# Kernel optimization log

Hardware: AMD Instinct MI355X
Metric: run time of the kernel (lower is better)

The kernel has to match this reference:

```python
import jax, jax.numpy as jnp
import numpy as np
from jax import lax

D, DIM, FF, V, B, S = 8, 1024, 4096, 32000, 2, 2048
EPS = 1e-6

def _rms(x, w):
    return x * lax.rsqrt(jnp.mean(x * x, axis=-1, keepdims=True) + EPS) * w

def _lin(x, W, b):
    # torch nn.Linear: weight [out, in]
    return x @ W.T + b

def _comb(e1, e2):
    # associative op for h_t = a_t * h_{t-1} + b_t  (h_0 = 0)
    a1, b1 = e1
    a2, b2 = e2
    return a1 * a2, a2 * b1 + b2

def _forward(tokens, emb, h0, Wf, bf, Wi, bi, Wig, big, Wog, bog, n1, n2, Wfc, bfc, Wfa, bfa, Wfo, bfo, nl, Wout, bout):
    # embedding with max_norm=1 renorm semantics
    e = emb[tokens]                                  # [B,S,DIM]
    nrm = jnp.linalg.norm(e, axis=-1, keepdims=True)
    x = jnp.where(nrm > 1.0, e / (nrm + 1e-7), e)
    for i in range(D):
        # --- QuasiLSTM sub-block ---
        x_ = x
        h_in = _rms(x, n1[i])
        f = jax.nn.sigmoid(_lin(h_in, Wf[i], bf[i]))                 # forget gate [B,S,DIM]
        v = jnp.tanh(_lin(h_in, Wi[i], bi[i])) * jax.nn.sigmoid(_lin(h_in, Wig[i], big[i]))
        _, h_inner = lax.associative_scan(_comb, (f, v), axis=1)     # inner-chunk scan (zero init)
        h = h_inner + h0[i][None, None, :] * jnp.cumprod(f, axis=1)  # cross-chunk from last_hidden_init
        y = jnp.tanh(h) * jax.nn.sigmoid(_lin(h_in, Wog[i], bog[i]))
        x = y + x_                                                   # dropout(p) is identity in eval
        # --- SwiGLU FFN sub-block ---
        x_ = x
        z = _rms(x, n2[i])
        u = _lin(z, Wfc[i], bfc[i]) * jax.nn.silu(_lin(z, Wfa[i], bfa[i]))
        x = _lin(u, Wfo[i], bfo[i]) + x_
    x = _rms(x, nl)
    return _lin(x, Wout, bout)                                       # [B,S,V]

def setup_inputs() -> dict:
    key = jax.random.key(0)
    ks = jax.random.split(key, 16)
    n = lambda k, s: jax.random.normal(k, s, jnp.float32) * 0.02
    zD = jnp.zeros((D, DIM), jnp.float32)
    return {
        "tokens": jax.random.randint(ks[0], (B, S), 0, V),
        "emb": n(ks[1], (V, DIM)),
        "h0": jax.random.normal(ks[2], (D, DIM), jnp.float32),
        "Wf": n(ks[3], (D, DIM, DIM)), "bf": zD,
        "Wi": n(ks[4], (D, DIM, DIM)), "bi": zD,
        "Wig": n(ks[5], (D, DIM, DIM)), "big": zD,
        "Wog": n(ks[6], (D, DIM, DIM)), "bog": zD,
        "n1": jnp.ones((D, DIM), jnp.float32),
        "n2": jnp.ones((D, DIM), jnp.float32),
        "Wfc": n(ks[7], (D, FF, DIM)), "bfc": jnp.zeros((D, FF), jnp.float32),
        "Wfa": n(ks[8], (D, FF, DIM)), "bfa": jnp.zeros((D, FF), jnp.float32),
        "Wfo": n(ks[9], (D, DIM, FF)), "bfo": zD,
        "nl": jnp.ones((DIM,), jnp.float32),
        "Wout": n(ks[10], (V, DIM)), "bout": jnp.zeros((V,), jnp.float32),
    }

def reference(tokens, emb, h0, Wf, bf, Wi, bi, Wig, big, Wog, bog, n1, n2, Wfc, bfc, Wfa, bfa, Wfo, bfo, nl, Wout, bout):
    return _forward(tokens, emb, h0, Wf, bf, Wi, bi, Wig, big, Wog, bog, n1, n2, Wfc, bfc, Wfa, bfa, Wfo, bfo, nl, Wout, bout)
```

## Files before the change

kernel.cpp:

```cpp
#include <hip/hip_runtime.h>
#include <hip/hip_bf16.h>
#include <cstdint>
#include <cstddef>

typedef unsigned short u16;
typedef __attribute__((ext_vector_type(4))) float f32x4;
typedef __attribute__((ext_vector_type(8))) short bf16x8;
typedef __attribute__((ext_vector_type(8))) unsigned short u16x8;
typedef __attribute__((ext_vector_type(4))) unsigned short u16x4;

#define D_LAYERS 8
#define DIMN 1024
#define FFD 4096
#define VOCAB 32000
#define MROWS 4096
#define SEQ 2048
#define NCHUNK 64
#define LCHUNK 32

__device__ __forceinline__ u16 f2b(float f) {
  union { float f; unsigned u; } v; v.f = f;
  unsigned r = v.u + 0x7FFFu + ((v.u >> 16) & 1u);
  return (u16)(r >> 16);
}
__device__ __forceinline__ float b2f(u16 h) {
  union { unsigned u; float f; } v; v.u = ((unsigned)h) << 16;
  return v.f;
}
__device__ __forceinline__ float sigm(float x) { return 1.f / (1.f + __expf(-x)); }
__device__ __forceinline__ float ftanh(float x) {
  float e = __expf(2.f * x);
  return 1.f - 2.f / (e + 1.f);
}

__device__ __forceinline__ void async16(const void* g, void* l) {
  auto gp = reinterpret_cast<const __attribute__((address_space(1))) char*>(
      reinterpret_cast<uintptr_t>(g));
  auto lp = reinterpret_cast<__attribute__((address_space(3))) char*>(
      reinterpret_cast<uintptr_t>(l));
  __builtin_amdgcn_global_load_lds(gp, lp, 16, 0, 0);
}

__device__ __forceinline__ float blk_sum(float v) {
  __shared__ float sm[4];
  #pragma unroll
  for (int o = 32; o > 0; o >>= 1) v += __shfl_xor(v, o);
  if ((threadIdx.x & 63) == 0) sm[threadIdx.x >> 6] = v;
  __syncthreads();
  float r = sm[0] + sm[1] + sm[2] + sm[3];
  __syncthreads();
  return r;
}

__global__ __launch_bounds__(256) void k_cvt(const f32x4* __restrict__ in,
                                             u16x8* __restrict__ out) {
  size_t i = (size_t)blockIdx.x * 256 + threadIdx.x;
  f32x4 a = in[i * 2], b = in[i * 2 + 1];
  u16x8 o;
  o[0] = f2b(a[0]); o[1] = f2b(a[1]); o[2] = f2b(a[2]); o[3] = f2b(a[3]);
  o[4] = f2b(b[0]); o[5] = f2b(b[1]); o[6] = f2b(b[2]); o[7] = f2b(b[3]);
  out[i] = o;
}

__global__ __launch_bounds__(256) void k_cvt7(
    const float* __restrict__ Wf, const float* __restrict__ Wi,
    const float* __restrict__ Wig, const float* __restrict__ Wog,
    const float* __restrict__ Wfc, const float* __restrict__ Wfa,
    const float* __restrict__ Wfo,
    u16* __restrict__ dGates,
    u16* __restrict__ dFc, u16* __restrict__ dFa, u16* __restrict__ dFo,
    int L)
{
  const int b = blockIdx.x;
  const float* src; u16* dst; size_t off;
  if (b < 2048) {
    const int g = b >> 9, r = b & 511;
    const float* s = (g == 0) ? Wf : (g == 1) ? Wi : (g == 2) ? Wig : Wog;
    src = s + (size_t)L * 1048576;
    dst = dGates + (size_t)g * 1048576;
    off = (size_t)r * 2048;
  } else if (b < 4096) {
    src = Wfc + (size_t)L * 4194304; dst = dFc; off = (size_t)(b - 2048) * 2048;
  } else if (b < 6144) {
    src = Wfa + (size_t)L * 4194304; dst = dFa; off = (size_t)(b - 4096) * 2048;
  } else {
    src = Wfo + (size_t)L * 4194304; dst = dFo; off = (size_t)(b - 6144) * 2048;
  }
  const size_t i = off + (size_t)threadIdx.x * 8;
  f32x4 a = *(const f32x4*)(src + i);
  f32x4 c = *(const f32x4*)(src + i + 4);
  u16x8 o;
  o[0] = f2b(a[0]); o[1] = f2b(a[1]); o[2] = f2b(a[2]); o[3] = f2b(a[3]);
  o[4] = f2b(c[0]); o[5] = f2b(c[1]); o[6] = f2b(c[2]); o[7] = f2b(c[3]);
  *(u16x8*)(dst + i) = o;
}

__global__ __launch_bounds__(256) void k_embed(const int* __restrict__ tok,
                                               const float* __restrict__ emb,
                                               float* __restrict__ x) {
  const int r = blockIdx.x;
  const int tk = tok[r];
  f32x4 v = ((const f32x4*)(emb + (size_t)tk * DIMN))[threadIdx.x];
  float ss = v[0]*v[0] + v[1]*v[1] + v[2]*v[2] + v[3]*v[3];
  float tot = blk_sum(ss);
  float nrm = sqrtf(tot);
  float s = (nrm > 1.f) ? (1.f / (nrm + 1e-7f)) : 1.f;
  f32x4 o = {v[0]*s, v[1]*s, v[2]*s, v[3]*s};
  ((f32x4*)(x + (size_t)r * DIMN))[threadIdx.x] = o;
}

__global__ __launch_bounds__(256) void k_rms(const float* __restrict__ x,
                                             const float* __restrict__ wgt,
                                             u16* __restrict__ out) {
  const int r = blockIdx.x;
  f32x4 v = ((const f32x4*)(x + (size_t)r * DIMN))[threadIdx.x];
  float ss = v[0]*v[0] + v[1]*v[1] + v[2]*v[2] + v[3]*v[3];
  float tot = blk_sum(ss);
  float sc = rsqrtf(tot * (1.f / DIMN) + 1e-6f);
  f32x4 w = ((const f32x4*)wgt)[threadIdx.x];
  u16x4 o;
  o[0] = f2b(v[0] * sc * w[0]);
  o[1] = f2b(v[1] * sc * w[1]);
  o[2] = f2b(v[2] * sc * w[2]);
  o[3] = f2b(v[3] * sc * w[3]);
  ((u16x4*)(out + (size_t)r * DIMN))[threadIdx.x] = o;
}

__global__ __launch_bounds__(256) void k_scanA(const float* __restrict__ f,
                                               const float* __restrict__ v,
                                               float* __restrict__ Ac,
                                               float* __restrict__ Vc) {
  const int bx = blockIdx.x;
  const int dg = bx & 3, c = (bx >> 2) & 63, b = bx >> 8;
  const int d = dg * 256 + threadIdx.x;
  const size_t base = ((size_t)(b * SEQ + c * LCHUNK)) * DIMN + d;
  float a = 1.f, h = 0.f;
  #pragma unroll 4
  for (int t = 0; t < LCHUNK; ++t) {
    size_t ix = base + (size_t)t * DIMN;
    float fv = f[ix];
    h = fv * h + v[ix];
    a *= fv;
  }
  const size_t ci = ((size_t)(b * NCHUNK + c)) * DIMN + d;
  Ac[ci] = a; Vc[ci] = h;
}

__global__ __launch_bounds__(256) void k_scanB(const float* __restrict__ Ac,
                                               const float* __restrict__ Vc,
                                               const float* __restrict__ h0,
                                               float* __restrict__ carry) {
  const int idx = blockIdx.x * 256 + threadIdx.x;
  const int b = idx >> 10, d = idx & 1023;
  float h = h0[d];
  for (int c = 0; c < NCHUNK; ++c) {
    size_t ci = ((size_t)(b * NCHUNK + c)) * DIMN + d;
    carry[ci] = h;
    h = Ac[ci] * h + Vc[ci];
  }
}

__global__ __launch_bounds__(256) void k_scanC(const float* __restrict__ f,
                                               const float* __restrict__ v,
                                               const float* __restrict__ oo,
                                               const float* __restrict__ carry,
                                               float* __restrict__ x) {
  const int bx = blockIdx.x;
  const int dg = bx & 3, c = (bx >> 2) & 63, b = bx >> 8;
  const int d = dg * 256 + threadIdx.x;
  const size_t base = ((size_t)(b * SEQ + c * LCHUNK)) * DIMN + d;
  float h = carry[((size_t)(b * NCHUNK + c)) * DIMN + d];
  for (int t = 0; t < LCHUNK; ++t) {
    size_t ix = base + (size_t)t * DIMN;
    float fv = f[ix];
    h = fv * h + v[ix];
    x[ix] += ftanh(h) * oo[ix];
  }
}

constexpr int EPI_SILU_BF = 1, EPI_MUL_BF = 2, EPI_RES_F32 = 3, EPI_BIAS_F32 = 4;

template<int BN_T, int EPI>
__global__ __launch_bounds__(256, 2)
void gemm_bt(const u16* __restrict__ A,
             const u16* __restrict__ B0,
             const float* __restrict__ bias0,
             float* __restrict__ oF0,
             u16* __restrict__ oB,
             const u16* __restrict__ exB, const float* __restrict__ exF,
             int N, int K)
{
  constexpr int MF = (BN_T == 128) ? 4 : 2;
  constexpr int WAVES_N = (BN_T == 128) ? 2 : 1;
  constexpr int ISS_B = BN_T / 32;
  __shared__ __align__(16) u16 As[128 * 64];
  __shared__ __align__(16) u16 Bs[BN_T * 64];
  const int tid = threadIdx.x;
  const int w = tid >> 6, lane = tid & 63;
  const int wm = w / WAVES_N, wn = w % WAVES_N;
  const int m0 = blockIdx.x * 128;
  const int n0 = blockIdx.y * BN_T;

  const u16* Bw = B0;
  const float* bias = bias0;
  float* oF = oF0;

  const f32x4 zero = {0.f, 0.f, 0.f, 0.f};
  f32x4 acc[MF][4];
  #pragma unroll
  for (int mf = 0; mf < MF; ++mf)
    #pragma unroll
    for (int nf = 0; nf < 4; ++nf) acc[mf][nf] = zero;

  for (int kt = 0; kt < K; kt += 64) {
    #pragma unroll
    for (int i = 0; i < 4; ++i) {
      int p = i * 4096 + w * 1024 + lane * 16;
      int r = p >> 7;
      int cs = (p & 127) ^ ((r & 7) << 4);
      async16(A + ((size_t)(m0 + r) * K + kt) + (cs >> 1),
              (char*)As + i * 4096 + w * 1024);
    }
    #pragma unroll
    for (int i = 0; i < ISS_B; ++i) {
      int p = i * 4096 + w * 1024 + lane * 16;
      int r = p >> 7;
      int cs = (p & 127) ^ ((r & 7) << 4);
      async16(Bw + ((size_t)(n0 + r) * K + kt) + (cs >> 1),
              (char*)Bs + i * 4096 + w * 1024);
    }
    __syncthreads();
    #pragma unroll
    for (int ks = 0; ks < 2; ++ks) {
      bf16x8 av[MF], bv[4];
      const int cbase = ks * 64 + ((lane >> 4) << 4);
      #pragma unroll
      for (int mf = 0; mf < MF; ++mf) {
        int r = wm * (MF * 16) + mf * 16 + (lane & 15);
        av[mf] = *(const bf16x8*)((const char*)As + r * 128 + (cbase ^ ((r & 7) << 4)));
      }
      #pragma unroll
      for (int nf = 0; nf < 4; ++nf) {
        int r = wn * 64 + nf * 16 + (lane & 15);
        bv[nf] = *(const bf16x8*)((const char*)Bs + r * 128 + (cbase ^ ((r & 7) << 4)));
      }
      #pragma unroll
      for (int mf = 0; mf < MF; ++mf)
        #pragma unroll
        for (int nf = 0; nf < 4; ++nf)
          acc[mf][nf] = __builtin_amdgcn_mfma_f32_16x16x32_bf16(
              av[mf], bv[nf], acc[mf][nf], 0, 0, 0);
    }
    __syncthreads();
  }

  #pragma unroll
  for (int nf = 0; nf < 4; ++nf) {
    const int n = n0 + wn * 64 + nf * 16 + (lane & 15);
    const float bb = bias[n];
    #pragma unroll
    for (int mf = 0; mf < MF; ++mf) {
      #pragma unroll
      for (int j = 0; j < 4; ++j) {
        const int m = m0 + wm * (MF * 16) + mf * 16 + ((lane >> 4) << 2) + j;
        const size_t idx = (size_t)m * N + n;
        float v = acc[mf][nf][j] + bb;
        if constexpr (EPI == EPI_SILU_BF) {
          oB[idx] = f2b(v * sigm(v));
        } else if constexpr (EPI == EPI_MUL_BF) {
          oB[idx] = f2b(v * b2f(exB[idx]));
        } else if constexpr (EPI == EPI_RES_F32) {
          oF[idx] = v + exF[idx];
        } else {
          oF[idx] = v;
        }
      }
    }
  }
}

constexpr int EDG = 0, EDF = 1;

template<int EPI>
__global__ __launch_bounds__(256, 2)
void gemm_dual(const u16* __restrict__ A,
               const u16* __restrict__ Ba0, const u16* __restrict__ Bb0,
               const u16* __restrict__ Ba1, const u16* __restrict__ Bb1,
               const float* __restrict__ ba0, const float* __restrict__ bb0,
               const float* __restrict__ ba1, const float* __restrict__ bb1,
               float* __restrict__ oV,
               float* __restrict__ oFa, float* __restrict__ oFb,
               u16* __restrict__ oU,
               int N, int K)
{
  __shared__ __align__(16) u16 As[128 * 64];
  __shared__ __align__(16) u16 Bsa[128 * 64];
  __shared__ __align__(16) u16 Bsb[128 * 64];
  const int tid = threadIdx.x;
  const int w = tid >> 6, lane = tid & 63;
  const int wm = w >> 1, wn = w & 1;
  const int m0 = blockIdx.x * 128;
  const int n0 = blockIdx.y * 128;
  const int z = blockIdx.z;

  const u16* Ba = (EPI == EDG && z) ? Ba1 : Ba0;
  const u16* Bb = (EPI == EDG && z) ? Bb1 : Bb0;
  const float* ba = (EPI == EDG && z) ? ba1 : ba0;
  const float* bb = (EPI == EDG && z) ? bb1 : bb0;

  const f32x4 zero = {0.f, 0.f, 0.f, 0.f};
  f32x4 accA[4][4], accB[4][4];
  #pragma unroll
  for (int mf = 0; mf < 4; ++mf)
    #pragma unroll
    for (int nf = 0; nf < 4; ++nf) { accA[mf][nf] = zero; accB[mf][nf] = zero; }

  for (int kt = 0; kt < K; kt += 64) {
    #pragma unroll
    for (int i = 0; i < 4; ++i) {
      const int p = i * 4096 + w * 1024 + lane * 16;
      const int r = p >> 7;
      const int cs = (p & 127) ^ ((r & 7) << 4);
      async16(A  + ((size_t)(m0 + r) * K + kt) + (cs >> 1),
              (char*)As + i * 4096 + w * 1024);
      async16(Ba + ((size_t)(n0 + r) * K + kt) + (cs >> 1),
              (char*)Bsa + i * 4096 + w * 1024);
      async16(Bb + ((size_t)(n0 + r) * K + kt) + (cs >> 1),
              (char*)Bsb + i * 4096 + w * 1024);
    }
    __syncthreads();
    #pragma unroll
    for (int ks = 0; ks < 2; ++ks) {
      bf16x8 av[4], bva[4], bvb[4];
      const int cbase = ks * 64 + ((lane >> 4) << 4);
      #pragma unroll
      for (int mf = 0; mf < 4; ++mf) {
        const int r = wm * 64 + mf * 16 + (lane & 15);
        av[mf] = *(const bf16x8*)((const char*)As + r * 128 + (cbase ^ ((r & 7) << 4)));
      }
      #pragma unroll
      for (int nf = 0; nf < 4; ++nf) {
        const int r = wn * 64 + nf * 16 + (lane & 15);
        const int off = r * 128 + (cbase ^ ((r & 7) << 4));
        bva[nf] = *(const bf16x8*)((const char*)Bsa + off);
        bvb[nf] = *(const bf16x8*)((const char*)Bsb + off);
      }
      #pragma unroll
      for (int mf = 0; mf < 4; ++mf)
        #pragma unroll
        for (int nf = 0; nf < 4; ++nf) {
          accA[mf][nf] = __builtin_amdgcn_mfma_f32_16x16x32_bf16(
              av[mf], bva[nf], accA[mf][nf], 0, 0, 0);
          accB[mf][nf] = __builtin_amdgcn_mfma_f32_16x16x32_bf16(
              av[mf], bvb[nf], accB[mf][nf], 0, 0, 0);
        }
    }
    __syncthreads();
  }

  #pragma unroll
  for (int nf = 0; nf < 4; ++nf) {
    const int n = n0 + wn * 64 + nf * 16 + (lane & 15);
    const float bba = ba[n], bbb = bb[n];
    #pragma unroll
    for (int mf = 0; mf < 4; ++mf) {
      #pragma unroll
      for (int j = 0; j < 4; ++j) {
        const int m = m0 + wm * 64 + mf * 16 + ((lane >> 4) << 2) + j;
        const size_t idx = (size_t)m * N + n;
        const float va = accA[mf][nf][j] + bba;
        const float vb = accB[mf][nf][j] + bbb;
        if constexpr (EPI == EDG) {
          if (z == 0) {
            oV[idx] = ftanh(va) * sigm(vb);
          } else {
            oFa[idx] = sigm(va);
            oFb[idx] = sigm(vb);
          }
        } else {
          oU[idx] = f2b(vb * va * sigm(va));
        }
      }
    }
  }
}

extern "C" void kernel_launch(void* const* d_in, const int* in_sizes, int n_in,
                              void* d_out, int out_size, void* d_ws, size_t ws_size,
                              hipStream_t stream) {
  (void)in_sizes; (void)n_in; (void)out_size; (void)ws_size;
  const int*   tokens = (const int*)d_in[0];
  const float* emb  = (const float*)d_in[1];
  const float* h0   = (const float*)d_in[2];
  const float* Wf   = (const float*)d_in[3];
  const float* bf_  = (const float*)d_in[4];
  const float* Wi   = (const float*)d_in[5];
  const float* bi_  = (const float*)d_in[6];
  const float* Wig  = (const float*)d_in[7];
  const float* big_ = (const float*)d_in[8];
  const float* Wog  = (const float*)d_in[9];
  const float* bog_ = (const float*)d_in[10];
  const float* n1   = (const float*)d_in[11];
  const float* n2   = (const float*)d_in[12];
  const float* Wfc  = (const float*)d_in[13];
  const float* bfc_ = (const float*)d_in[14];
  const float* Wfa  = (const float*)d_in[15];
  const float* bfa_ = (const float*)d_in[16];
  const float* Wfo  = (const float*)d_in[17];
  const float* bfo_ = (const float*)d_in[18];
  const float* nl_  = (const float*)d_in[19];
  const float* Wout = (const float*)d_in[20];
  const float* bout_= (const float*)d_in[21];
  float* out = (float*)d_out;

  char* p = (char*)d_ws;
  auto alloc = [&](size_t bytes) {
    char* r = p; p += (bytes + 255) & ~(size_t)255; return r;
  };
  u16* wbGates = (u16*)alloc((size_t)4 * DIMN * DIMN * 2);
  u16* wbWfc  = (u16*)alloc((size_t)FFD * DIMN * 2);
  u16* wbWfa  = (u16*)alloc((size_t)FFD * DIMN * 2);
  u16* wbWfo  = (u16*)alloc((size_t)FFD * DIMN * 2);
  u16* wbWout = (u16*)alloc((size_t)VOCAB * DIMN * 2);
  float* x    = (float*)alloc((size_t)MROWS * DIMN * 4);
  u16* hin    = (u16*)alloc((size_t)MROWS * DIMN * 2);
  float* fbuf = (float*)alloc((size_t)MROWS * DIMN * 4);
  float* vbuf = (float*)alloc((size_t)MROWS * DIMN * 4);
  float* oobuf= (float*)alloc((size_t)MROWS * DIMN * 4);
  u16* ub     = (u16*)alloc((size_t)MROWS * FFD * 2);
  float* Ac    = (float*)alloc((size_t)2 * NCHUNK * DIMN * 4);
  float* Vc    = (float*)alloc((size_t)2 * NCHUNK * DIMN * 4);
  float* carry = (float*)alloc((size_t)2 * NCHUNK * DIMN * 4);

  u16* wbWf  = wbGates;
  u16* wbWi  = wbGates + (size_t)1 * DIMN * DIMN;
  u16* wbWig = wbGates + (size_t)2 * DIMN * DIMN;
  u16* wbWog = wbGates + (size_t)3 * DIMN * DIMN;

  k_embed<<<dim3(MROWS), dim3(256), 0, stream>>>(tokens, emb, x);

  for (int L = 0; L < D_LAYERS; ++L) {
    k_cvt7<<<dim3(8192), dim3(256), 0, stream>>>(
        Wf, Wi, Wig, Wog, Wfc, Wfa, Wfo,
        wbGates, wbWfc, wbWfa, wbWfo, L);

    k_rms<<<dim3(MROWS), dim3(256), 0, stream>>>(x, n1 + (size_t)L * DIMN, hin);

    gemm_dual<EDG><<<dim3(32, 8, 2), dim3(256), 0, stream>>>(
        hin, wbWi, wbWig, wbWf, wbWog,
        bi_ + (size_t)L * DIMN, big_ + (size_t)L * DIMN,
        bf_ + (size_t)L * DIMN, bog_ + (size_t)L * DIMN,
        vbuf, fbuf, oobuf, nullptr, DIMN, DIMN);

    k_scanA<<<dim3(512), dim3(256), 0, stream>>>(fbuf, vbuf, Ac, Vc);
    k_scanB<<<dim3(8), dim3(256), 0, stream>>>(Ac, Vc, h0 + (size_t)L * DIMN, carry);
    k_scanC<<<dim3(512), dim3(256), 0, stream>>>(fbuf, vbuf, oobuf, carry, x);

    k_rms<<<dim3(MROWS), dim3(256), 0, stream>>>(x, n2 + (size_t)L * DIMN, hin);

    gemm_dual<EDF><<<dim3(32, 32, 1), dim3(256), 0, stream>>>(
        hin, wbWfa, wbWfc, nullptr, nullptr,
        bfa_ + (size_t)L * FFD, bfc_ + (size_t)L * FFD, nullptr, nullptr,
        nullptr, nullptr, nullptr, ub, FFD, DIMN);

    gemm_bt<64, EPI_RES_F32><<<dim3(32, 16), dim3(256), 0, stream>>>(
        ub, wbWfo,
        bfo_ + (size_t)L * DIMN,
        x, nullptr, nullptr, x, DIMN, FFD);
  }

  k_cvt<<<dim3(16000), dim3(256), 0, stream>>>((const f32x4*)Wout, (u16x8*)wbWout);
  k_rms<<<dim3(MROWS), dim3(256), 0, stream>>>(x, nl_, hin);
  gemm_bt<128, EPI_BIAS_F32><<<dim3(32, 250), dim3(256), 0, stream>>>(
      hin, wbWout,
      bout_,
      out, nullptr, nullptr, nullptr, VOCAB, DIMN);
}
```

Baseline: 2.139 ms.

## Split-K the FFN down-projection and swizzle GEMM block order for cache locality

The FFN output GEMM (K=4096) becomes a split-K with two halves on 128x128 tiles, writing fp32 partials. A new reduction kernel then sums the partials with the bias and the residual into x. All GEMM launches now use a 1D grid whose block index is remapped across groups of 8, so that blocks sharing the same A and B tiles run closer together for L2 or MALL reuse. The cost is an extra 32MB partial buffer written and read back in each layer, plus one extra kernel launch per layer.

```diff
diff --git a/kernel.cpp b/kernel.cpp
--- a/kernel.cpp
+++ b/kernel.cpp
@@ -178,7 +178,21 @@
   }
 }
 
-constexpr int EPI_SILU_BF = 1, EPI_MUL_BF = 2, EPI_RES_F32 = 3, EPI_BIAS_F32 = 4;
+__global__ __launch_bounds__(256) void k_red(const f32x4* __restrict__ pp,
+                                             const float* __restrict__ bias,
+                                             float* __restrict__ x) {
+  const size_t i = (size_t)blockIdx.x * 256 + threadIdx.x;
+  const int n4 = (int)(i & 255);
+  f32x4 a = pp[i];
+  f32x4 b = pp[i + (size_t)MROWS * DIMN / 4];
+  f32x4 bs = ((const f32x4*)bias)[n4];
+  f32x4 xv = ((const f32x4*)x)[i];
+  f32x4 o = {xv[0] + a[0] + b[0] + bs[0], xv[1] + a[1] + b[1] + bs[1],
+             xv[2] + a[2] + b[2] + bs[2], xv[3] + a[3] + b[3] + bs[3]};
+  ((f32x4*)x)[i] = o;
+}
+
+constexpr int EPI_BIAS_F32 = 4, EPI_PART = 5;
 
 template<int BN_T, int EPI>
 __global__ __launch_bounds__(256, 2)
@@ -186,9 +200,7 @@
              const u16* __restrict__ B0,
              const float* __restrict__ bias0,
              float* __restrict__ oF0,
-             u16* __restrict__ oB,
-             const u16* __restrict__ exB, const float* __restrict__ exF,
-             int N, int K)
+             int N, int K, int LD, int GX)
 {
   constexpr int MF = (BN_T == 128) ? 4 : 2;
   constexpr int WAVES_N = (BN_T == 128) ? 2 : 1;
@@ -198,12 +210,20 @@
   const int tid = threadIdx.x;
   const int w = tid >> 6, lane = tid & 63;
   const int wm = w / WAVES_N, wn = w % WAVES_N;
-  const int m0 = blockIdx.x * 128;
-  const int n0 = blockIdx.y * BN_T;
-
+  const int bid = blockIdx.x;
+  const int q = (int)gridDim.x >> 3;
+  const int swz = (bid & 7) * q + (bid >> 3);
+  const int m0 = (swz % GX) * 128;
+  const int n0 = (swz / GX) * BN_T;
+
+  const u16* Aw = A;
   const u16* Bw = B0;
-  const float* bias = bias0;
   float* oF = oF0;
+  if constexpr (EPI == EPI_PART) {
+    const int koff = blockIdx.z * K;
+    Aw += koff; Bw += koff;
+    oF += (size_t)blockIdx.z * MROWS * DIMN;
+  }
 
   const f32x4 zero = {0.f, 0.f, 0.f, 0.f};
   f32x4 acc[MF][4];
@@ -218,7 +238,7 @@
       int p = i * 4096 + w * 1024 + lane * 16;
       int r = p >> 7;
       int cs = (p & 127) ^ ((r & 7) << 4);
-      async16(A + ((size_t)(m0 + r) * K + kt) + (cs >> 1),
+      async16(Aw + ((size_t)(m0 + r) * LD + kt) + (cs >> 1),
               (char*)As + i * 4096 + w * 1024);
     }
     #pragma unroll
@@ -226,7 +246,7 @@
       int p = i * 4096 + w * 1024 + lane * 16;
       int r = p >> 7;
       int cs = (p & 127) ^ ((r & 7) << 4);
-      async16(Bw + ((size_t)(n0 + r) * K + kt) + (cs >> 1),
+      async16(Bw + ((size_t)(n0 + r) * LD + kt) + (cs >> 1),
               (char*)Bs + i * 4096 + w * 1024);
     }
     __syncthreads();
@@ -257,23 +277,14 @@
   #pragma unroll
   for (int nf = 0; nf < 4; ++nf) {
     const int n = n0 + wn * 64 + nf * 16 + (lane & 15);
-    const float bb = bias[n];
+    const float bb = (EPI == EPI_PART) ? 0.f : bias0[n];
     #pragma unroll
     for (int mf = 0; mf < MF; ++mf) {
       #pragma unroll
       for (int j = 0; j < 4; ++j) {
         const int m = m0 + wm * (MF * 16) + mf * 16 + ((lane >> 4) << 2) + j;
         const size_t idx = (size_t)m * N + n;
-        float v = acc[mf][nf][j] + bb;
-        if constexpr (EPI == EPI_SILU_BF) {
-          oB[idx] = f2b(v * sigm(v));
-        } else if constexpr (EPI == EPI_MUL_BF) {
-          oB[idx] = f2b(v * b2f(exB[idx]));
-        } else if constexpr (EPI == EPI_RES_F32) {
-          oF[idx] = v + exF[idx];
-        } else {
-          oF[idx] = v;
-        }
+        oF[idx] = acc[mf][nf][j] + bb;
       }
     }
   }
@@ -291,7 +302,7 @@
                float* __restrict__ oV,
                float* __restrict__ oFa, float* __restrict__ oFb,
                u16* __restrict__ oU,
-               int N, int K)
+               int N, int K, int GX)
 {
   __shared__ __align__(16) u16 As[128 * 64];
   __shared__ __align__(16) u16 Bsa[128 * 64];
@@ -299,9 +310,12 @@
   const int tid = threadIdx.x;
   const int w = tid >> 6, lane = tid & 63;
   const int wm = w >> 1, wn = w & 1;
-  const int m0 = blockIdx.x * 128;
-  const int n0 = blockIdx.y * 128;
-  const int z = blockIdx.z;
+  const int bid = blockIdx.x;
+  const int q = (int)gridDim.x >> 3;
+  const int swz = (bid & 7) * q + (bid >> 3);
+  const int m0 = (swz % GX) * 128;
+  const int n0 = (swz / GX) * 128;
+  const int z = blockIdx.y;
 
   const u16* Ba = (EPI == EDG && z) ? Ba1 : Ba0;
   const u16* Bb = (EPI == EDG && z) ? Bb1 : Bb0;
@@ -428,6 +442,7 @@
   float* vbuf = (float*)alloc((size_t)MROWS * DIMN * 4);
   float* oobuf= (float*)alloc((size_t)MROWS * DIMN * 4);
   u16* ub     = (u16*)alloc((size_t)MROWS * FFD * 2);
+  float* pk   = (float*)alloc((size_t)2 * MROWS * DIMN * 4);
   float* Ac    = (float*)alloc((size_t)2 * NCHUNK * DIMN * 4);
   float* Vc    = (float*)alloc((size_t)2 * NCHUNK * DIMN * 4);
   float* carry = (float*)alloc((size_t)2 * NCHUNK * DIMN * 4);
@@ -446,11 +461,11 @@
 
     k_rms<<<dim3(MROWS), dim3(256), 0, stream>>>(x, n1 + (size_t)L * DIMN, hin);
 
-    gemm_dual<EDG><<<dim3(32, 8, 2), dim3(256), 0, stream>>>(
+    gemm_dual<EDG><<<dim3(256, 2), dim3(256), 0, stream>>>(
         hin, wbWi, wbWig, wbWf, wbWog,
         bi_ + (size_t)L * DIMN, big_ + (size_t)L * DIMN,
         bf_ + (size_t)L * DIMN, bog_ + (size_t)L * DIMN,
-        vbuf, fbuf, oobuf, nullptr, DIMN, DIMN);
+        vbuf, fbuf, oobuf, nullptr, DIMN, DIMN, 32);
 
     k_scanA<<<dim3(512), dim3(256), 0, stream>>>(fbuf, vbuf, Ac, Vc);
     k_scanB<<<dim3(8), dim3(256), 0, stream>>>(Ac, Vc, h0 + (size_t)L * DIMN, carry);
@@ -458,21 +473,19 @@
 
     k_rms<<<dim3(MROWS), dim3(256), 0, stream>>>(x, n2 + (size_t)L * DIMN, hin);
 
-    gemm_dual<EDF><<<dim3(32, 32, 1), dim3(256), 0, stream>>>(
+    gemm_dual<EDF><<<dim3(1024, 1), dim3(256), 0, stream>>>(
         hin, wbWfa, wbWfc, nullptr, nullptr,
         bfa_ + (size_t)L * FFD, bfc_ + (size_t)L * FFD, nullptr, nullptr,
-        nullptr, nullptr, nullptr, ub, FFD, DIMN);
-
-    gemm_bt<64, EPI_RES_F32><<<dim3(32, 16), dim3(256), 0, stream>>>(
-        ub, wbWfo,
-        bfo_ + (size_t)L * DIMN,
-        x, nullptr, nullptr, x, DIMN, FFD);
+        nullptr, nullptr, nullptr, ub, FFD, DIMN, 32);
+
+    gemm_bt<128, EPI_PART><<<dim3(256, 1, 2), dim3(256), 0, stream>>>(
+        ub, wbWfo, nullptr, pk, DIMN, FFD / 2, FFD, 32);
+    k_red<<<dim3(MROWS), dim3(256), 0, stream>>>(
+        (const f32x4*)pk, bfo_ + (size_t)L * DIMN, x);
   }
 
   k_cvt<<<dim3(16000), dim3(256), 0, stream>>>((const f32x4*)Wout, (u16x8*)wbWout);
   k_rms<<<dim3(MROWS), dim3(256), 0, stream>>>(x, nl_, hin);
-  gemm_bt<128, EPI_BIAS_F32><<<dim3(32, 250), dim3(256), 0, stream>>>(
-      hin, wbWout,
-      bout_,
-      out, nullptr, nullptr, nullptr, VOCAB, DIMN);
-}
+  gemm_bt<128, EPI_BIAS_F32><<<dim3(8000), dim3(256), 0, stream>>>(
+      hin, wbWout, bout_, out, VOCAB, DIMN, DIMN, 32);
+}
```

Measured after the change: 2.268 ms. +6.0%, slower.
